# Optimization experiments

Hardware: AMD Instinct MI355X
Metric: run time of the kernel (lower is better)

The kernel has to match this reference:

```python
import jax, jax.numpy as jnp
import numpy as np

P, Q = 4, 16            # mlp_quad_last_shape
N, D_IN, H = 100000, 3, 256
N_QUAD = 128


def setup_inputs() -> dict:
    key = jax.random.key(0)
    ks = jax.random.split(key, 20)
    sc = lambda fan: 1.0 / np.sqrt(fan)
    inp = {}
    inp["input"] = jax.random.normal(ks[0], (N, D_IN), jnp.float32)
    inp["eq_param"] = jax.random.uniform(ks[1], (1,), jnp.float32)
    for i in range(5):
        inp[f"quad_x{i}"] = jax.random.uniform(ks[2 + i], (N_QUAD, 1), jnp.float32)
    # mlp_x params: Linear(3->256) -> tanh -> Linear(256->1024=P^5)
    inp["Wx1"] = jax.random.normal(ks[7], (D_IN, H), jnp.float32) * sc(D_IN)
    inp["bx1"] = jnp.zeros((H,), jnp.float32)
    inp["Wx2"] = jax.random.normal(ks[8], (H, P ** 5), jnp.float32) * sc(H)
    inp["bx2"] = jnp.zeros((P ** 5,), jnp.float32)
    # per-axis quad MLPs: Linear(1 -> P*Q)
    for i in range(5):
        inp[f"Wq{i}"] = jax.random.normal(ks[9 + i], (1, P * Q), jnp.float32) * sc(1)
        inp[f"bq{i}"] = jnp.zeros((P * Q,), jnp.float32)
    return inp


def reference(input, eq_param, quad_x0, quad_x1, quad_x2, quad_x3, quad_x4,
              Wx1, bx1, Wx2, bx2,
              Wq0, bq0, Wq1, bq1, Wq2, bq2, Wq3, bq3, Wq4, bq4):
    # lhs = mlp_x(input): [N, P^5]
    lhs = jnp.tanh(input @ Wx1 + bx1) @ Wx2 + bx2

    quads = (quad_x0, quad_x1, quad_x2, quad_x3, quad_x4)
    Ws = (Wq0, Wq1, Wq2, Wq3, Wq4)
    bs = (bq0, bq1, bq2, bq3, bq4)

    # Each factor: out_quad_i = y_i * (quad_x_i @ Wq_i + bq_i), reshape [n_i, P, Q].
    # The original einsum 'abx,cdx,efx,lmx,wvx->abcdeflmwv' followed by movedims,
    # reshape and sum over the merged n-axes is a multilinear map, so summing
    # each factor over its n_i axis FIRST gives the identical rhs tensor
    # (sum commutes with the outer product), avoiding the 10-D intermediate.
    ss = []
    for qx, W, b in zip(quads, Ws, bs):
        y = jnp.exp(-jnp.sum(qx * qx, axis=-1, keepdims=True) * eq_param[0])  # r_func weight [n_i,1]
        oq = (y * (qx @ W + b)).reshape(-1, P, Q)  # [n_i, P, Q]
        ss.append(jnp.sum(oq, axis=0))             # [P, Q]
    s0, s1, s2, s3, s4 = ss
    # rhs[b,d,f,m,v] = sum_x s0[b,x] s1[d,x] s2[f,x] s3[m,x] s4[v,x]  -> flatten to [P^5]
    rhs = jnp.einsum('bx,dx,fx,mx,vx->bdfmv', s0, s1, s2, s3, s4).reshape(-1)
    return lhs @ rhs  # [N]
```

## Files before the change

### kernel.cpp

```cpp
#include <hip/hip_runtime.h>

#define QQ 16
#define NQ 128
#define HH 256
#define P5 1024
#define LOG2E   1.44269504088896340f
#define K2LOG2E 2.88539008177792681f
#define RPT 7

__device__ __forceinline__ float fast_exp2(float x) {
  return __builtin_amdgcn_exp2f(x);
}

__device__ __forceinline__ float block_sum256(float v, float* red, int t) {
#pragma unroll
  for (int o = 32; o > 0; o >>= 1) v += __shfl_down(v, o, 64);
  if ((t & 63) == 0) red[t >> 6] = v;
  __syncthreads();
  float r = red[0] + red[1] + red[2] + red[3];
  __syncthreads();
  return r;
}

__global__ __launch_bounds__(256) void prep_kernel(
    const float* __restrict__ eq,
    const float* __restrict__ q0, const float* __restrict__ q1,
    const float* __restrict__ q2, const float* __restrict__ q3,
    const float* __restrict__ q4,
    const float* __restrict__ Wx1, const float* __restrict__ bx1,
    const float* __restrict__ Wx2, const float* __restrict__ bx2,
    const float* __restrict__ Wq0, const float* __restrict__ bq0,
    const float* __restrict__ Wq1, const float* __restrict__ bq1,
    const float* __restrict__ Wq2, const float* __restrict__ bq2,
    const float* __restrict__ Wq3, const float* __restrict__ bq3,
    const float* __restrict__ Wq4, const float* __restrict__ bq4,
    float* __restrict__ ws) {
  __shared__ float sS[5][64];
  __shared__ float sRhs[P5];
  __shared__ float sPart[4][10];
  __shared__ float sAB[10];
  __shared__ float red[4];

  const int t = threadIdx.x;
  const int hb = blockIdx.x;
  const float c = -eq[0] * LOG2E;

  const float* qs[5]  = {q0, q1, q2, q3, q4};
  const float* Wqs[5] = {Wq0, Wq1, Wq2, Wq3, Wq4};
  const float* bqs[5] = {bq0, bq1, bq2, bq3, bq4};

  float v[10];
#pragma unroll
  for (int i = 0; i < 5; ++i) {
    float a = 0.f, b = 0.f;
    if (t < NQ) {
      float x = qs[i][t];
      float y = fast_exp2(x * x * c);
      a = y * x;
      b = y;
    }
    v[2 * i] = a;
    v[2 * i + 1] = b;
  }
#pragma unroll
  for (int k = 0; k < 10; ++k) {
    float s = v[k];
#pragma unroll
    for (int o = 32; o > 0; o >>= 1) s += __shfl_down(s, o, 64);
    if ((t & 63) == 0) sPart[t >> 6][k] = s;
  }
  __syncthreads();
  if (t < 10) sAB[t] = sPart[0][t] + sPart[1][t] + sPart[2][t] + sPart[3][t];
  __syncthreads();

  for (int k = t; k < 5 * 64; k += 256) {
    int i = k >> 6, j = k & 63;
    sS[i][j] = Wqs[i][j] * sAB[2 * i] + bqs[i][j] * sAB[2 * i + 1];
  }
  __syncthreads();

  for (int idx = t; idx < P5; idx += 256) {
    int b = (idx >> 8) & 3, d = (idx >> 6) & 3, f = (idx >> 4) & 3,
        m = (idx >> 2) & 3, w = idx & 3;
    float s = 0.f;
#pragma unroll
    for (int x = 0; x < QQ; ++x)
      s += sS[0][b * QQ + x] * sS[1][d * QQ + x] * sS[2][f * QQ + x] *
           sS[3][m * QQ + x] * sS[4][w * QQ + x];
    sRhs[idx] = s;
  }
  __syncthreads();

  const float* wrow = Wx2 + hb * P5;
  float p = 0.f;
#pragma unroll
  for (int k = 0; k < 4; ++k)
    p = fmaf(wrow[t + 256 * k], sRhs[t + 256 * k], p);
  p = block_sum256(p, red, t);

  if (t == 0) {
    ws[hb]          = K2LOG2E * Wx1[hb];
    ws[HH + hb]     = K2LOG2E * Wx1[HH + hb];
    ws[2 * HH + hb] = K2LOG2E * Wx1[2 * HH + hb];
    ws[3 * HH + hb] = K2LOG2E * bx1[hb];
    ws[4 * HH + hb] = -2.0f * p;
  }

  if (hb == 0) {
    float pb = 0.f;
    for (int j = t; j < P5; j += 256) pb = fmaf(bx2[j], sRhs[j], pb);
    pb = block_sum256(pb, red, t);
    if (t == 0) ws[5 * HH] = pb;
  }
}

__global__ __launch_bounds__(256) void main_kernel(
    const float* __restrict__ input, const float* __restrict__ ws,
    float* __restrict__ out, int n) {
  __shared__ float4 qtab[HH];
  __shared__ float4 wtab4[HH / 4];
  __shared__ float red[4];
  __shared__ float sred[4][RPT][64];

  const int t = threadIdx.x;
  const int lane = t & 63;
  const int wv = t >> 6;

  const float w0 = ws[t], w1 = ws[HH + t], w2 = ws[2 * HH + t];
  const float bb = ws[3 * HH + t], wr = ws[4 * HH + t];
  qtab[t] = make_float4(w0, w1, w2, bb);
  ((float*)wtab4)[t] = wr;

  float s = wr;
#pragma unroll
  for (int o = 32; o > 0; o >>= 1) s += __shfl_xor(s, o, 64);
  if (lane == 0) red[wv] = s;
  __syncthreads();
  const float CONST = fmaf(-0.5f, (red[0] + red[1]) + (red[2] + red[3]),
                           ws[5 * HH]);

  const int row0 = blockIdx.x * (RPT * 64);
  float x0[RPT], x1[RPT], x2[RPT], acc[RPT];
#pragma unroll
  for (int r = 0; r < RPT; ++r) {
    const int row = row0 + r * 64 + lane;
    x0[r] = x1[r] = x2[r] = 0.f;
    if (row < n) {
      x0[r] = input[row * 3 + 0];
      x1[r] = input[row * 3 + 1];
      x2[r] = input[row * 3 + 2];
    }
    acc[r] = 0.f;
  }

  const int hbase = wv * 64;
#pragma unroll 4
  for (int j = 0; j < 16; ++j) {
    const float4 wq = wtab4[wv * 16 + j];
    const float wrv[4] = {wq.x, wq.y, wq.z, wq.w};
#pragma unroll
    for (int u = 0; u < 4; ++u) {
      const float4 q = qtab[hbase + j * 4 + u];
#pragma unroll
      for (int r = 0; r < RPT; ++r) {
        float a = fmaf(q.z, x2[r], fmaf(q.y, x1[r], fmaf(q.x, x0[r], q.w)));
        float rc = __builtin_amdgcn_rcpf(fast_exp2(a) + 1.0f);
        acc[r] = fmaf(wrv[u], rc, acc[r]);
      }
    }
  }

#pragma unroll
  for (int r = 0; r < RPT; ++r) sred[wv][r][lane] = acc[r];
  __syncthreads();

  for (int rr = wv; rr < RPT; rr += 4) {
    const int row = row0 + rr * 64 + lane;
    if (row < n) {
      float sum = (sred[0][rr][lane] + sred[1][rr][lane]) +
                  (sred[2][rr][lane] + sred[3][rr][lane]);
      out[row] = sum + CONST;
    }
  }
}

extern "C" void kernel_launch(void* const* d_in, const int* in_sizes, int n_in,
                              void* d_out, int out_size, void* d_ws,
                              size_t ws_size, hipStream_t stream) {
  const float* input = (const float*)d_in[0];
  const float* eq    = (const float*)d_in[1];
  const float* q0    = (const float*)d_in[2];
  const float* q1    = (const float*)d_in[3];
  const float* q2    = (const float*)d_in[4];
  const float* q3    = (const float*)d_in[5];
  const float* q4    = (const float*)d_in[6];
  const float* Wx1   = (const float*)d_in[7];
  const float* bx1   = (const float*)d_in[8];
  const float* Wx2   = (const float*)d_in[9];
  const float* bx2   = (const float*)d_in[10];
  const float* Wq0   = (const float*)d_in[11];
  const float* bq0   = (const float*)d_in[12];
  const float* Wq1   = (const float*)d_in[13];
  const float* bq1   = (const float*)d_in[14];
  const float* Wq2   = (const float*)d_in[15];
  const float* bq2   = (const float*)d_in[16];
  const float* Wq3   = (const float*)d_in[17];
  const float* bq3   = (const float*)d_in[18];
  const float* Wq4   = (const float*)d_in[19];
  const float* bq4   = (const float*)d_in[20];

  float* ws  = (float*)d_ws;
  float* out = (float*)d_out;
  const int n = in_sizes[0] / 3;

  hipLaunchKernelGGL(prep_kernel, dim3(HH), dim3(256), 0, stream,
                     eq, q0, q1, q2, q3, q4, Wx1, bx1, Wx2, bx2,
                     Wq0, bq0, Wq1, bq1, Wq2, bq2, Wq3, bq3, Wq4, bq4, ws);

  const int rows_per_block = RPT * 64;
  const int blocks = (n + rows_per_block - 1) / rows_per_block;
  hipLaunchKernelGGL(main_kernel, dim3(blocks), dim3(256), 0, stream,
                     input, ws, out, n);
}
```

Baseline: 113.8 us.

## Split hidden units across eight waves and factor rhs outer-product computation

The main kernel now runs 512-thread blocks of eight waves, each covering 32 hidden units instead of 64, and each block handles 4 row-groups of 64 rows instead of 7. Partial sums from all eight waves are reduced through shared memory. This spreads the work over more blocks and waves, at the cost of a larger cross-wave reduction and more per-block setup. In the prep kernel, each thread now computes four rhs entries while sharing the product of the other four factors, which removes redundant multiplies.

```diff
diff --git a/kernel.cpp b/kernel.cpp
--- a/kernel.cpp
+++ b/kernel.cpp
@@ -6,7 +6,7 @@
 #define P5 1024
 #define LOG2E   1.44269504088896340f
 #define K2LOG2E 2.88539008177792681f
-#define RPT 7
+#define RPT 4
 
 __device__ __forceinline__ float fast_exp2(float x) {
   return __builtin_amdgcn_exp2f(x);
@@ -79,15 +79,20 @@
   }
   __syncthreads();
 
-  for (int idx = t; idx < P5; idx += 256) {
-    int b = (idx >> 8) & 3, d = (idx >> 6) & 3, f = (idx >> 4) & 3,
-        m = (idx >> 2) & 3, w = idx & 3;
-    float s = 0.f;
-#pragma unroll
-    for (int x = 0; x < QQ; ++x)
-      s += sS[0][b * QQ + x] * sS[1][d * QQ + x] * sS[2][f * QQ + x] *
-           sS[3][m * QQ + x] * sS[4][w * QQ + x];
-    sRhs[idx] = s;
+  {
+    const int d = (t >> 6) & 3, f = (t >> 4) & 3, m = (t >> 2) & 3,
+              vv = t & 3;
+    float s[4] = {0.f, 0.f, 0.f, 0.f};
+#pragma unroll
+    for (int x = 0; x < QQ; ++x) {
+      const float c1 = sS[1][d * QQ + x] * sS[2][f * QQ + x];
+      const float c2 = sS[3][m * QQ + x] * sS[4][vv * QQ + x];
+      const float cc = c1 * c2;
+#pragma unroll
+      for (int b = 0; b < 4; ++b) s[b] = fmaf(sS[0][b * QQ + x], cc, s[b]);
+    }
+#pragma unroll
+    for (int b = 0; b < 4; ++b) sRhs[b * 256 + t] = s[b];
   }
   __syncthreads();
 
@@ -114,27 +119,28 @@
   }
 }
 
-__global__ __launch_bounds__(256) void main_kernel(
+__global__ __launch_bounds__(512) void main_kernel(
     const float* __restrict__ input, const float* __restrict__ ws,
     float* __restrict__ out, int n) {
   __shared__ float4 qtab[HH];
   __shared__ float4 wtab4[HH / 4];
   __shared__ float red[4];
-  __shared__ float sred[4][RPT][64];
+  __shared__ float sred[8][RPT][64];
 
   const int t = threadIdx.x;
   const int lane = t & 63;
   const int wv = t >> 6;
 
-  const float w0 = ws[t], w1 = ws[HH + t], w2 = ws[2 * HH + t];
-  const float bb = ws[3 * HH + t], wr = ws[4 * HH + t];
-  qtab[t] = make_float4(w0, w1, w2, bb);
-  ((float*)wtab4)[t] = wr;
-
-  float s = wr;
-#pragma unroll
-  for (int o = 32; o > 0; o >>= 1) s += __shfl_xor(s, o, 64);
-  if (lane == 0) red[wv] = s;
+  if (t < HH) {
+    const float w0 = ws[t], w1 = ws[HH + t], w2 = ws[2 * HH + t];
+    const float bb = ws[3 * HH + t], wr = ws[4 * HH + t];
+    qtab[t] = make_float4(w0, w1, w2, bb);
+    ((float*)wtab4)[t] = wr;
+    float s = wr;
+#pragma unroll
+    for (int o = 32; o > 0; o >>= 1) s += __shfl_xor(s, o, 64);
+    if (lane == 0) red[wv] = s;
+  }
   __syncthreads();
   const float CONST = fmaf(-0.5f, (red[0] + red[1]) + (red[2] + red[3]),
                            ws[5 * HH]);
@@ -153,10 +159,10 @@
     acc[r] = 0.f;
   }
 
-  const int hbase = wv * 64;
+  const int hbase = wv * 32;
 #pragma unroll 4
-  for (int j = 0; j < 16; ++j) {
-    const float4 wq = wtab4[wv * 16 + j];
+  for (int j = 0; j < 8; ++j) {
+    const float4 wq = wtab4[wv * 8 + j];
     const float wrv[4] = {wq.x, wq.y, wq.z, wq.w};
 #pragma unroll
     for (int u = 0; u < 4; ++u) {
@@ -174,11 +180,14 @@
   for (int r = 0; r < RPT; ++r) sred[wv][r][lane] = acc[r];
   __syncthreads();
 
-  for (int rr = wv; rr < RPT; rr += 4) {
+  if (t < 256) {
+    const int rr = t >> 6;
     const int row = row0 + rr * 64 + lane;
     if (row < n) {
-      float sum = (sred[0][rr][lane] + sred[1][rr][lane]) +
-                  (sred[2][rr][lane] + sred[3][rr][lane]);
+      float sum = ((sred[0][rr][lane] + sred[1][rr][lane]) +
+                   (sred[2][rr][lane] + sred[3][rr][lane])) +
+                  ((sred[4][rr][lane] + sred[5][rr][lane]) +
+                   (sred[6][rr][lane] + sred[7][rr][lane]));
       out[row] = sum + CONST;
     }
   }
@@ -219,6 +228,6 @@
 
   const int rows_per_block = RPT * 64;
   const int blocks = (n + rows_per_block - 1) / rows_per_block;
-  hipLaunchKernelGGL(main_kernel, dim3(blocks), dim3(256), 0, stream,
+  hipLaunchKernelGGL(main_kernel, dim3(blocks), dim3(512), 0, stream,
                      input, ws, out, n);
 }
```

After: 111.7 us. No clear change (-1.9%).
